# Kernel tuning notes

Hardware: AMD Instinct MI355X
Metric: run time of the kernel (lower is better)

## Reference

```python
import jax, jax.numpy as jnp
import numpy as np

WIN = 7
SHIFT = 3
HEADS = 12
DIM = 384
HID = 4 * DIM
B, H, W = 32, 56, 56
N = WIN * WIN  # window area
EPS = 1e-5


def _rel_pos_index():
    coords = np.stack(np.meshgrid(np.arange(WIN), np.arange(WIN), indexing='ij'))  # (2,7,7)
    flat = coords.reshape(2, -1)  # (2,49)
    rel = flat[:, :, None] - flat[:, None, :]  # (2,49,49)
    rel = rel.transpose(1, 2, 0)
    rel[:, :, 0] += WIN - 1
    rel[:, :, 1] += WIN - 1
    rel[:, :, 0] *= 2 * WIN - 1
    return rel.sum(-1)  # (49,49) indices into (2*7-1)^2=169 table


def _attn_mask():
    img = np.zeros((H, W), dtype=np.float32)
    hs = [(0, H - WIN), (H - WIN, H - SHIFT), (H - SHIFT, H)]
    ws = [(0, W - WIN), (W - WIN, W - SHIFT), (W - SHIFT, W)]
    cnt = 0
    for h0, h1 in hs:
        for w0, w1 in ws:
            img[h0:h1, w0:w1] = cnt
            cnt += 1
    mw = img.reshape(H // WIN, WIN, W // WIN, WIN).transpose(0, 2, 1, 3).reshape(-1, N)  # (nW,49)
    d = mw[:, None, :] - mw[:, :, None]
    return np.where(d != 0, -100.0, 0.0).astype(np.float32)  # (nW,49,49)


_RPI = jnp.asarray(_rel_pos_index())
_MASK = jnp.asarray(_attn_mask())


def _ln(t, w, b):
    m = t.mean(-1, keepdims=True)
    v = ((t - m) ** 2).mean(-1, keepdims=True)
    return (t - m) * jax.lax.rsqrt(v + EPS) * w + b


def setup_inputs() -> dict:
    key = jax.random.key(0)
    ks = jax.random.split(key, 16)
    s = 0.02
    return {
        'x': jax.random.normal(ks[0], (B, H, W, DIM), jnp.float32),
        'norm1_w': jnp.ones((DIM,), jnp.float32),
        'norm1_b': jnp.zeros((DIM,), jnp.float32),
        'qkv_w': jax.random.normal(ks[1], (3 * DIM, DIM), jnp.float32) * s,
        'qkv_b': jnp.zeros((3 * DIM,), jnp.float32),
        'rel_bias_table': jax.random.normal(ks[2], ((2 * WIN - 1) ** 2, HEADS), jnp.float32) * s,
        'proj_w': jax.random.normal(ks[3], (DIM, DIM), jnp.float32) * s,
        'proj_b': jnp.zeros((DIM,), jnp.float32),
        'norm2_w': jnp.ones((DIM,), jnp.float32),
        'norm2_b': jnp.zeros((DIM,), jnp.float32),
        'fc1_w': jax.random.normal(ks[4], (HID, DIM), jnp.float32) * s,
        'fc1_b': jnp.zeros((HID,), jnp.float32),
        'fc2_w': jax.random.normal(ks[5], (DIM, HID), jnp.float32) * s,
        'fc2_b': jnp.zeros((DIM,), jnp.float32),
    }


def reference(x, norm1_w, norm1_b, qkv_w, qkv_b, rel_bias_table, proj_w, proj_b,
              norm2_w, norm2_b, fc1_w, fc1_b, fc2_w, fc2_b):
    Bt, Ht, Wt, C = x.shape
    hd = C // HEADS
    nh, nw = Ht // WIN, Wt // WIN
    nWtot = nh * nw

    # ---- attention branch ----
    h = _ln(x, norm1_w, norm1_b)
    h = jnp.roll(h, (-SHIFT, -SHIFT), axis=(1, 2))
    # window partition -> (B*nW, N, C)
    hw = h.reshape(Bt, nh, WIN, nw, WIN, C).transpose(0, 1, 3, 2, 4, 5).reshape(-1, N, C)
    qkv = hw @ qkv_w.T + qkv_b  # (B_, N, 3C)
    qkv = qkv.reshape(-1, N, 3, HEADS, hd).transpose(2, 0, 3, 1, 4)
    q, k, v = qkv[0], qkv[1], qkv[2]  # (B_, heads, N, hd)
    scale = hd ** -0.5
    attn = jnp.einsum('bhnd,bhmd->bhnm', q * scale, k)
    bias = rel_bias_table[_RPI].transpose(2, 0, 1)  # (heads, N, N)
    attn = attn + bias[None]
    attn = attn.reshape(Bt, nWtot, HEADS, N, N) + _MASK[None, :, None]
    attn = jax.nn.softmax(attn, axis=-1).reshape(-1, HEADS, N, N)
    o = jnp.einsum('bhnm,bhmd->bhnd', attn, v)
    o = o.transpose(0, 2, 1, 3).reshape(-1, N, C)
    o = o @ proj_w.T + proj_b
    # window reverse + roll back
    o = o.reshape(Bt, nh, nw, WIN, WIN, C).transpose(0, 1, 3, 2, 4, 5).reshape(Bt, Ht, Wt, C)
    o = jnp.roll(o, (SHIFT, SHIFT), axis=(1, 2))
    x = x + o

    # ---- MLP branch ----
    h = _ln(x, norm2_w, norm2_b)
    h = jax.nn.gelu(h @ fc1_w.T + fc1_b, approximate=False)
    h = h @ fc2_w.T + fc2_b
    return x + h
```

## Files before the change

### kernel.cpp

```cpp
#include <hip/hip_runtime.h>
#include <hip/hip_bf16.h>
#include <math.h>

using bf16 = __hip_bfloat16;
typedef short bf16x8 __attribute__((ext_vector_type(8)));
typedef float f32x4 __attribute__((ext_vector_type(4)));

static constexpr int  TOK     = 100352;
static constexpr long QKV_SEG = 38535168L;

__device__ __forceinline__ float bf2f(short u) {
    return __uint_as_float(((unsigned)(unsigned short)u) << 16);
}
__device__ __forceinline__ short f2bs(float x) {
    unsigned u = __float_as_uint(x);
    u += 0x7FFF + ((u >> 16) & 1);
    return (short)(u >> 16);
}
__device__ __forceinline__ void gload16(const void* g, void* l) {
    __builtin_amdgcn_global_load_lds(
        (const __attribute__((address_space(1))) unsigned int*)g,
        (__attribute__((address_space(3))) unsigned int*)l, 16, 0, 0);
}
__device__ __forceinline__ float gelu_fast(float x) {
    const float x2 = x * x;
    const float t1 = x * x2;
    const float y  = fmaf(0.071354816222f, t1, 1.5957691216f * x);
    const float e  = __expf(-y);
    return x * __frcp_rn(1.f + e);
}

__global__ __launch_bounds__(256)
void convert_w_kernel(const float* __restrict__ qkv_w, const float* __restrict__ proj_w,
                      const float* __restrict__ fc1_w, const float* __restrict__ fc2_w,
                      bf16* __restrict__ out)
{
    const int i4 = (blockIdx.x * 256 + threadIdx.x) * 4;
    if (i4 >= 1769472) return;
    const float* src; int off;
    if (i4 < 442368)       { src = qkv_w;  off = i4; }
    else if (i4 < 589824)  { src = proj_w; off = i4 - 442368; }
    else if (i4 < 1179648) { src = fc1_w;  off = i4 - 589824; }
    else                   { src = fc2_w;  off = i4 - 1179648; }
    const float4 v = *(const float4*)&src[off];
    out[i4+0] = __float2bfloat16(v.x);
    out[i4+1] = __float2bfloat16(v.y);
    out[i4+2] = __float2bfloat16(v.z);
    out[i4+3] = __float2bfloat16(v.w);
}

template<bool WINDOWED>
__global__ __launch_bounds__(256)
void ln_kernel(const float* __restrict__ x, const float* __restrict__ gw,
               const float* __restrict__ gb, bf16* __restrict__ out)
{
    const int wave = threadIdx.x >> 6;
    const int lane = threadIdx.x & 63;
    const long t = (long)blockIdx.x * 4 + wave;
    size_t src;
    if (WINDOWED) {
        int bb = (int)(t / 3136); int rem = (int)(t - (long)bb * 3136);
        int wIdx = rem / 49;      int n = rem - wIdx * 49;
        int wh = wIdx >> 3, ww = wIdx & 7;
        int yi = n / 7,     xi = n - yi * 7;
        int r = wh * 7 + yi + 3; if (r >= 56) r -= 56;
        int c = ww * 7 + xi + 3; if (c >= 56) c -= 56;
        src = ((size_t)bb * 3136 + (size_t)r * 56 + c) * 384;
    } else {
        src = (size_t)t * 384;
    }
    float v[6]; float s = 0.f, sq = 0.f;
    #pragma unroll
    for (int kk = 0; kk < 6; ++kk) {
        v[kk] = x[src + lane + 64 * kk];
        s += v[kk]; sq += v[kk] * v[kk];
    }
    #pragma unroll
    for (int o = 32; o > 0; o >>= 1) { s += __shfl_xor(s, o); sq += __shfl_xor(sq, o); }
    const float m   = s * (1.f / 384.f);
    const float var = sq * (1.f / 384.f) - m * m;
    const float rs  = rsqrtf(var + 1e-5f);
    #pragma unroll
    for (int kk = 0; kk < 6; ++kk) {
        int ch = lane + 64 * kk;
        out[(size_t)t * 384 + ch] = __float2bfloat16((v[kk] - m) * rs * gw[ch] + gb[ch]);
    }
}

template<int MODE>
__global__ __launch_bounds__(256)
void gemm_bt(const bf16* __restrict__ A, const bf16* __restrict__ W,
             const float* __restrict__ bias, bf16* __restrict__ outb,
             float* __restrict__ outf, const float* __restrict__ resid,
             int K, int tilesN)
{
    __shared__ bf16 As[128 * 64];
    __shared__ bf16 Bs[128 * 64];
    const int nwg = gridDim.x;
    const int b0  = blockIdx.x;
    const int swz = (b0 & 7) * (nwg >> 3) + (b0 >> 3);
    const int tm = swz / tilesN;
    const int tn = swz - tm * tilesN;
    const int tid  = threadIdx.x;
    const int lane = tid & 63;
    const int wid  = tid >> 6;
    const int wr = (wid >> 1) * 64;
    const int wc = (wid & 1) * 64;
    const int sr = tid >> 3;
    const int sc = (tid & 7) * 8;
    const int scs = sc ^ ((sr & 7) << 3);

    f32x4 acc[4][4];
    #pragma unroll
    for (int i = 0; i < 4; ++i)
        #pragma unroll
        for (int j = 0; j < 4; ++j) acc[i][j] = (f32x4)0.0f;

    const long am0 = (long)tm * 128;
    const int  bn0 = tn * 128;
    const bf16* Ab = A + am0 * K + scs;
    const bf16* Wb = W + (long)bn0 * K + scs;

    const int rophase = (lane & 7) << 3;
    const int kbase   = (lane >> 4) * 8;

    for (int k0 = 0; k0 < K; k0 += 64) {
        #pragma unroll
        for (int p = 0; p < 4; ++p) {
            const int row = p * 32 + sr;
            gload16(&Ab[(size_t)row * K + k0], &As[row * 64 + sc]);
            gload16(&Wb[(size_t)row * K + k0], &Bs[row * 64 + sc]);
        }
        __syncthreads();
        #pragma unroll
        for (int kk = 0; kk < 2; ++kk) {
            const int kofs = (kk * 32 + kbase) ^ rophase;
            bf16x8 aF[4], bF[4];
            #pragma unroll
            for (int mi = 0; mi < 4; ++mi)
                aF[mi] = *(const bf16x8*)&As[(wr + mi * 16 + (lane & 15)) * 64 + kofs];
            #pragma unroll
            for (int ni = 0; ni < 4; ++ni)
                bF[ni] = *(const bf16x8*)&Bs[(wc + ni * 16 + (lane & 15)) * 64 + kofs];
            #pragma unroll
            for (int ni = 0; ni < 4; ++ni)
                #pragma unroll
                for (int mi = 0; mi < 4; ++mi)
                    acc[ni][mi] = __builtin_amdgcn_mfma_f32_16x16x32_bf16(
                        bF[ni], aF[mi], acc[ni][mi], 0, 0, 0);
        }
        __syncthreads();
    }

    const int g4 = (lane >> 4) << 2;
    int    gn0c[4];
    float4 bvc[4];
    #pragma unroll
    for (int nf = 0; nf < 4; ++nf) {
        gn0c[nf] = bn0 + wc + nf * 16 + g4;
        bvc[nf]  = *(const float4*)&bias[gn0c[nf]];
    }

    #pragma unroll
    for (int mf = 0; mf < 4; ++mf) {
        const long gm = am0 + wr + mf * 16 + (lane & 15);
        size_t tokdst = 0;
        long wwi = 0; int ntok = 0;
        if (MODE == 0) {
            wwi = gm / 49; ntok = (int)(gm - wwi * 49);
        } else if (MODE == 1) {
            int bb = (int)(gm / 3136); int rem = (int)(gm - (long)bb * 3136);
            int wIdx = rem / 49; int n = rem - wIdx * 49;
            int wh = wIdx >> 3, ww2 = wIdx & 7;
            int yi = n / 7,     xi = n - yi * 7;
            int rr = wh * 7 + yi + 3; if (rr >= 56) rr -= 56;
            int cc = ww2 * 7 + xi + 3; if (cc >= 56) cc -= 56;
            tokdst = ((size_t)bb * 3136 + (size_t)rr * 56 + cc) * 384;
        }
        #pragma unroll
        for (int nf = 0; nf < 4; ++nf) {
            const int gn0 = gn0c[nf];
            float vals[4];
            #pragma unroll
            for (int r = 0; r < 4; ++r) vals[r] = acc[nf][mf][r] + ((const float*)&bvc[nf])[r];

            if (MODE == 0) {
                const int s3 = gn0 / 384; const int rem = gn0 - s3 * 384;
                const int hh = rem >> 5, d0 = rem & 31;
                size_t dst = (size_t)s3 * QKV_SEG
                           + ((size_t)(wwi * 12 + hh) * 49 + ntok) * 32 + d0;
                union { short h4[4]; uint2 u2; } pk;
                if (s3 == 0) {
                    #pragma unroll
                    for (int r = 0; r < 4; ++r)
                        pk.h4[r] = f2bs(vals[r] * 0.17677669529663687f);
                } else {
                    #pragma unroll
                    for (int r = 0; r < 4; ++r) pk.h4[r] = f2bs(vals[r]);
                }
                *(uint2*)&outb[dst] = pk.u2;
            } else if (MODE == 1) {
                size_t dst = tokdst + gn0;
                const float4 rv = *(const float4*)&resid[dst];
                float4 ov;
                ov.x = rv.x + vals[0]; ov.y = rv.y + vals[1];
                ov.z = rv.z + vals[2]; ov.w = rv.w + vals[3];
                *(float4*)&outf[dst] = ov;
            } else if (MODE == 2) {
                union { short h4[4]; uint2 u2; } pk;
                #pragma unroll
                for (int r = 0; r < 4; ++r) pk.h4[r] = f2bs(gelu_fast(vals[r]));
                *(uint2*)&outb[(size_t)gm * 1536 + gn0] = pk.u2;
            } else {
                size_t dst = (size_t)gm * 384 + gn0;
                const float4 rv = *(const float4*)&resid[dst];
                float4 ov;
                ov.x = rv.x + vals[0]; ov.y = rv.y + vals[1];
                ov.z = rv.z + vals[2]; ov.w = rv.w + vals[3];
                *(float4*)&outf[dst] = ov;
            }
        }
    }
}

__global__ __launch_bounds__(256)
void attn_mfma(const bf16* __restrict__ q, const bf16* __restrict__ k,
               const bf16* __restrict__ v, const float* __restrict__ table,
               bf16* __restrict__ o)
{
    __shared__ bf16  vt_s[4][2048];
    __shared__ bf16  p_s[4][4096];
    __shared__ float tbl_s[4][169];

    const int tid  = threadIdx.x;
    const int wid  = tid >> 6;
    const int lane = tid & 63;
    const int li = lane & 15, g = lane >> 4;
    const int gwh = blockIdx.x * 4 + wid;
    const int w = gwh / 12, h = gwh - w * 12;
    const int wIdx = w & 63;
    const int bh = wIdx >> 3, bw = wIdx & 7;
    const size_t base = (size_t)gwh * 1568;

    char* vt = (char*)vt_s[wid];
    char* ps = (char*)p_s[wid];

    for (int t = lane; t < 169; t += 64) tbl_s[wid][t] = table[t * 12 + h];

    {
        const int4 z = {0, 0, 0, 0};
        #pragma unroll
        for (int t = 0; t < 4; ++t) ((int4*)vt)[t * 64 + lane] = z;
        for (int t = lane; t < 196; t += 64) {
            const int j = t >> 2, d0 = (t & 3) * 8;
            bf16x8 row = *(const bf16x8*)&v[base + (size_t)j * 32 + d0];
            #pragma unroll
            for (int u = 0; u < 8; ++u) {
                const int d = d0 + u;
                int off = (d << 7) + (j << 1);
                off ^= (d & 7) << 4;
                *(short*)(vt + off) = row[u];
            }
        }
    }

    bf16x8 aK[4], bQ[4];
    const int koff = g * 8;
    #pragma unroll
    for (int mj = 0; mj < 4; ++mj)
        aK[mj] = *(const bf16x8*)&k[base + (size_t)(mj * 16 + li) * 32 + koff];
    #pragma unroll
    for (int ni = 0; ni < 4; ++ni)
        bQ[ni] = *(const bf16x8*)&q[base + (size_t)(ni * 16 + li) * 32 + koff];

    f32x4 acc[4][4];
    #pragma unroll
    for (int i = 0; i < 4; ++i)
        #pragma unroll
        for (int j = 0; j < 4; ++j) acc[i][j] = (f32x4)0.0f;
    #pragma unroll
    for (int mj = 0; mj < 4; ++mj)
        #pragma unroll
        for (int ni = 0; ni < 4; ++ni)
            acc[mj][ni] = __builtin_amdgcn_mfma_f32_16x16x32_bf16(
                aK[mj], bQ[ni], acc[mj][ni], 0, 0, 0);

    const bool bndH = (bh == 7), bndW = (bw == 7);
    #pragma unroll
    for (int ni = 0; ni < 4; ++ni) {
        const int i = ni * 16 + li;
        const int yi = i / 7, xi = i - yi * 7;
        const int ri = (bndH ? (yi < 4 ? 3 : 6) : 0) + (bndW ? (xi < 4 ? 1 : 2) : 0);
        float mx = -1e30f;
        #pragma unroll
        for (int mj = 0; mj < 4; ++mj)
            #pragma unroll
            for (int r = 0; r < 4; ++r) {
                const int j = mj * 16 + g * 4 + r;
                const int yj = j / 7, xj = j - yj * 7;
                int ridx = (yi - yj + 6) * 13 + (xi - xj + 6);
                ridx = max(0, min(168, ridx));
                float val = acc[mj][ni][r] + tbl_s[wid][ridx];
                const int rj = (bndH ? (yj < 4 ? 3 : 6) : 0) + (bndW ? (xj < 4 ? 1 : 2) : 0);
                if (ri != rj) val -= 100.f;
                if (j >= 49) val = -1e30f;
                acc[mj][ni][r] = val;
                mx = fmaxf(mx, val);
            }
        mx = fmaxf(mx, __shfl_xor(mx, 16));
        mx = fmaxf(mx, __shfl_xor(mx, 32));
        float sum = 0.f;
        #pragma unroll
        for (int mj = 0; mj < 4; ++mj)
            #pragma unroll
            for (int r = 0; r < 4; ++r) {
                const float p = __expf(acc[mj][ni][r] - mx);
                acc[mj][ni][r] = p; sum += p;
            }
        sum += __shfl_xor(sum, 16);
        sum += __shfl_xor(sum, 32);
        const float inv = 1.f / sum;
        #pragma unroll
        for (int mj = 0; mj < 4; ++mj) {
            union { short h4[4]; uint2 u2; } pk;
            #pragma unroll
            for (int r = 0; r < 4; ++r) pk.h4[r] = f2bs(acc[mj][ni][r] * inv);
            int off = (i << 7) + ((mj * 16 + g * 4) << 1);
            off ^= (i & 7) << 4;
            *(uint2*)(ps + off) = pk.u2;
        }
    }

    f32x4 acc2[2][4];
    #pragma unroll
    for (int i = 0; i < 2; ++i)
        #pragma unroll
        for (int j = 0; j < 4; ++j) acc2[i][j] = (f32x4)0.0f;
    #pragma unroll
    for (int kk = 0; kk < 2; ++kk) {
        bf16x8 aV[2], bP[4];
        #pragma unroll
        for (int md = 0; md < 2; ++md) {
            const int d = md * 16 + li;
            int off = (d << 7) + kk * 64 + g * 16;
            off ^= (d & 7) << 4;
            aV[md] = *(const bf16x8*)(vt + off);
        }
        #pragma unroll
        for (int ni = 0; ni < 4; ++ni) {
            const int i = ni * 16 + li;
            int off = (i << 7) + kk * 64 + g * 16;
            off ^= (i & 7) << 4;
            bP[ni] = *(const bf16x8*)(ps + off);
        }
        #pragma unroll
        for (int md = 0; md < 2; ++md)
            #pragma unroll
            for (int ni = 0; ni < 4; ++ni)
                acc2[md][ni] = __builtin_amdgcn_mfma_f32_16x16x32_bf16(
                    aV[md], bP[ni], acc2[md][ni], 0, 0, 0);
    }

    const size_t obase = (size_t)w * 49 * 384 + h * 32;
    #pragma unroll
    for (int ni = 0; ni < 4; ++ni) {
        const int i = ni * 16 + li;
        if (i < 49) {
            #pragma unroll
            for (int md = 0; md < 2; ++md) {
                const int d0 = md * 16 + g * 4;
                union { short h4[4]; uint2 u2; } pk;
                #pragma unroll
                for (int r = 0; r < 4; ++r) pk.h4[r] = f2bs(acc2[md][ni][r]);
                *(uint2*)&o[obase + (size_t)i * 384 + d0] = pk.u2;
            }
        }
    }
}

extern "C" void kernel_launch(void* const* d_in, const int* in_sizes, int n_in,
                              void* d_out, int out_size, void* d_ws, size_t ws_size,
                              hipStream_t stream) {
    const float* x      = (const float*)d_in[0];
    const float* n1w    = (const float*)d_in[1];
    const float* n1b    = (const float*)d_in[2];
    const float* qkv_w  = (const float*)d_in[3];
    const float* qkv_b  = (const float*)d_in[4];
    const float* table  = (const float*)d_in[5];
    const float* proj_w = (const float*)d_in[6];
    const float* proj_b = (const float*)d_in[7];
    const float* n2w    = (const float*)d_in[8];
    const float* n2b    = (const float*)d_in[9];
    const float* fc1_w  = (const float*)d_in[10];
    const float* fc1_b  = (const float*)d_in[11];
    const float* fc2_w  = (const float*)d_in[12];
    const float* fc2_b  = (const float*)d_in[13];
    float* out = (float*)d_out;

    char* ws = (char*)d_ws;
    bf16* buf0 = (bf16*)ws;
    bf16* buf1 = (bf16*)(ws + 77070336);
    bf16* wb   = (bf16*)(ws + 77070336 + 308281344);

    convert_w_kernel<<<1728, 256, 0, stream>>>(qkv_w, proj_w, fc1_w, fc2_w, wb);
    ln_kernel<true><<<TOK / 4, 256, 0, stream>>>(x, n1w, n1b, buf0);
    gemm_bt<0><<<784 * 9, 256, 0, stream>>>(buf0, wb, qkv_b,
                                            buf1, nullptr, nullptr, 384, 9);
    attn_mfma<<<2048 * 12 / 4, 256, 0, stream>>>(buf1, buf1 + QKV_SEG,
                                                 buf1 + 2 * QKV_SEG, table, buf0);
    gemm_bt<1><<<784 * 3, 256, 0, stream>>>(buf0, wb + 442368, proj_b,
                                            nullptr, out, x, 384, 3);
    ln_kernel<false><<<TOK / 4, 256, 0, stream>>>(out, n2w, n2b, buf0);
    gemm_bt<2><<<784 * 12, 256, 0, stream>>>(buf0, wb + 589824, fc1_b,
                                             buf1, nullptr, nullptr, 384, 12);
    gemm_bt<3><<<784 * 3, 256, 0, stream>>>(buf1, wb + 1179648, fc2_b,
                                            nullptr, out, out, 1536, 3);
}
```

Measured before the change: 959.1 us.

## Enlarge GEMM tile to 256x128 with 512-thread blocks and compile-time K

The GEMM kernel now uses 8 waves per block covering a 256x128 output tile instead of 4 waves on 128x128, so each staged weight tile feeds twice as many rows. K becomes a template parameter so loop bounds are known at compile time, and index math moves to 32-bit ints. GELU uses a raw v_rcp_f32 instead of a correctly rounded reciprocal. The tradeoffs are more LDS per block, which may lower occupancy, and slightly lower GELU accuracy.

Measured after the change: 814.6 us (median of 4 runs). 15.1% less time.

```diff
diff --git a/kernel.cpp b/kernel.cpp
--- a/kernel.cpp
+++ b/kernel.cpp
@@ -16,6 +16,11 @@
     unsigned u = __float_as_uint(x);
     u += 0x7FFF + ((u >> 16) & 1);
     return (short)(u >> 16);
+}
+__device__ __forceinline__ float fast_rcp(float x) {
+    float r;
+    asm volatile("v_rcp_f32 %0, %1" : "=v"(r) : "v"(x));
+    return r;
 }
 __device__ __forceinline__ void gload16(const void* g, void* l) {
     __builtin_amdgcn_global_load_lds(
@@ -27,7 +32,7 @@
     const float t1 = x * x2;
     const float y  = fmaf(0.071354816222f, t1, 1.5957691216f * x);
     const float e  = __expf(-y);
-    return x * __frcp_rn(1.f + e);
+    return x * fast_rcp(1.f + e);
 }
 
 __global__ __launch_bounds__(256)
@@ -87,14 +92,14 @@
     }
 }
 
-template<int MODE>
-__global__ __launch_bounds__(256)
+template<int MODE, int K>
+__global__ __launch_bounds__(512)
 void gemm_bt(const bf16* __restrict__ A, const bf16* __restrict__ W,
              const float* __restrict__ bias, bf16* __restrict__ outb,
              float* __restrict__ outf, const float* __restrict__ resid,
-             int K, int tilesN)
+             int tilesN)
 {
-    __shared__ bf16 As[128 * 64];
+    __shared__ bf16 As[256 * 64];
     __shared__ bf16 Bs[128 * 64];
     const int nwg = gridDim.x;
     const int b0  = blockIdx.x;
@@ -104,8 +109,8 @@
     const int tid  = threadIdx.x;
     const int lane = tid & 63;
     const int wid  = tid >> 6;
-    const int wr = (wid >> 1) * 64;
-    const int wc = (wid & 1) * 64;
+    const int wr = (wid >> 1) << 6;
+    const int wc = (wid & 1) << 6;
     const int sr = tid >> 3;
     const int sc = (tid & 7) * 8;
     const int scs = sc ^ ((sr & 7) << 3);
@@ -116,10 +121,10 @@
         #pragma unroll
         for (int j = 0; j < 4; ++j) acc[i][j] = (f32x4)0.0f;
 
-    const long am0 = (long)tm * 128;
-    const int  bn0 = tn * 128;
-    const bf16* Ab = A + am0 * K + scs;
-    const bf16* Wb = W + (long)bn0 * K + scs;
+    const int am0 = tm * 256;
+    const int bn0 = tn * 128;
+    const bf16* Ab = A + (size_t)am0 * K + scs;
+    const bf16* Wb = W + (size_t)bn0 * K + scs;
 
     const int rophase = (lane & 7) << 3;
     const int kbase   = (lane >> 4) * 8;
@@ -127,8 +132,12 @@
     for (int k0 = 0; k0 < K; k0 += 64) {
         #pragma unroll
         for (int p = 0; p < 4; ++p) {
-            const int row = p * 32 + sr;
+            const int row = p * 64 + sr;
             gload16(&Ab[(size_t)row * K + k0], &As[row * 64 + sc]);
+        }
+        #pragma unroll
+        for (int p = 0; p < 2; ++p) {
+            const int row = p * 64 + sr;
             gload16(&Wb[(size_t)row * K + k0], &Bs[row * 64 + sc]);
         }
         __syncthreads();
@@ -163,13 +172,13 @@
 
     #pragma unroll
     for (int mf = 0; mf < 4; ++mf) {
-        const long gm = am0 + wr + mf * 16 + (lane & 15);
+        const int gm = am0 + wr + mf * 16 + (lane & 15);
         size_t tokdst = 0;
-        long wwi = 0; int ntok = 0;
+        int wwi = 0, ntok = 0;
         if (MODE == 0) {
-            wwi = gm / 49; ntok = (int)(gm - wwi * 49);
+            wwi = gm / 49; ntok = gm - wwi * 49;
         } else if (MODE == 1) {
-            int bb = (int)(gm / 3136); int rem = (int)(gm - (long)bb * 3136);
+            int bb = gm / 3136; int rem = gm - bb * 3136;
             int wIdx = rem / 49; int n = rem - wIdx * 49;
             int wh = wIdx >> 3, ww2 = wIdx & 7;
             int yi = n / 7,     xi = n - yi * 7;
@@ -404,15 +413,15 @@
 
     convert_w_kernel<<<1728, 256, 0, stream>>>(qkv_w, proj_w, fc1_w, fc2_w, wb);
     ln_kernel<true><<<TOK / 4, 256, 0, stream>>>(x, n1w, n1b, buf0);
-    gemm_bt<0><<<784 * 9, 256, 0, stream>>>(buf0, wb, qkv_b,
-                                            buf1, nullptr, nullptr, 384, 9);
+    gemm_bt<0, 384><<<392 * 9, 512, 0, stream>>>(buf0, wb, qkv_b,
+                                                 buf1, nullptr, nullptr, 9);
     attn_mfma<<<2048 * 12 / 4, 256, 0, stream>>>(buf1, buf1 + QKV_SEG,
                                                  buf1 + 2 * QKV_SEG, table, buf0);
-    gemm_bt<1><<<784 * 3, 256, 0, stream>>>(buf0, wb + 442368, proj_b,
-                                            nullptr, out, x, 384, 3);
+    gemm_bt<1, 384><<<392 * 3, 512, 0, stream>>>(buf0, wb + 442368, proj_b,
+                                                 nullptr, out, x, 3);
     ln_kernel<false><<<TOK / 4, 256, 0, stream>>>(out, n2w, n2b, buf0);
-    gemm_bt<2><<<784 * 12, 256, 0, stream>>>(buf0, wb + 589824, fc1_b,
-                                             buf1, nullptr, nullptr, 384, 12);
-    gemm_bt<3><<<784 * 3, 256, 0, stream>>>(buf1, wb + 1179648, fc2_b,
-                                            nullptr, out, out, 1536, 3);
-}
+    gemm_bt<2, 384><<<392 * 12, 512, 0, stream>>>(buf0, wb + 589824, fc1_b,
+                                                  buf1, nullptr, nullptr, 12);
+    gemm_bt<3, 1536><<<392 * 3, 512, 0, stream>>>(buf1, wb + 1179648, fc2_b,
+                                                  nullptr, out, out, 3);
+}
```
